# Optimization experiments

Measured on AMD Instinct MI355X. Metric: run time of the kernel, lower is better.

Reference implementation:

```python
import jax, jax.numpy as jnp
import numpy as np
from jax import lax

EPS = 2.220446049250313e-16  # np.finfo(float).eps, as in the torch source
DN3 = ('NCDHW', 'OIDHW', 'NCDHW')
DN2 = ('NCHW', 'OIHW', 'NCHW')


def setup_inputs() -> dict:
    key = jax.random.key(0)
    k1, k2, k3 = jax.random.split(key, 3)
    x = jax.random.normal(k1, (256, 256), dtype=jnp.float32)
    filts_temp = jax.random.normal(k2, (8, 1, 2, 9, 9), dtype=jnp.float32)    # [Ft,1,T=2,kh,kw]
    filts_notemp = jax.random.normal(k3, (8, 1, 1, 9, 9), dtype=jnp.float32)  # [Fn,1,1,kh,kw]
    return {"x": x, "filts_temp": filts_temp, "filts_notemp": filts_notemp, "num_rfs": 2}


def _forward(x, filts_temp, filts_notemp, num_rfs):
    kh, kw = filts_temp.shape[3], filts_temp.shape[4]
    corr_x = num_rfs * kh  # torch uses shape[3]
    corr_y = num_rfs * kw  # torch uses shape[4]
    num_filts = filts_temp.shape[0] + filts_notemp.shape[0]

    # x -> [1,1,2,H,W]: duplicate the frame along a temporal axis of length 2
    xv = jnp.broadcast_to(x, (2,) + x.shape)[None, None]

    # fixed-filter temporal conv3d + ReLU (halved)
    x_temp = jax.nn.relu(
        lax.conv_general_dilated(xv, filts_temp, (1, 1, 1), 'VALID', dimension_numbers=DN3) / 2
    )  # [1,Ft,1,H',W']
    # non-temporal conv on the last time slice
    x_notemp = jax.nn.relu(
        lax.conv_general_dilated(xv[:, :, -1:, :, :], filts_notemp, (1, 1, 1), 'VALID',
                                 dimension_numbers=DN3)
    )  # [1,Fn,1,H',W']

    xc = jnp.concatenate([x_temp, x_notemp], axis=1)  # [1,nf,1,H',W']
    # normalize across the filter channel (divisive normalization)
    x1 = xc / (jnp.sum(xc, axis=1, keepdims=True) + EPS)

    H_, W_ = x1.shape[3], x1.shape[4]
    x1f = x1[0, :, 0]  # [nf,H',W']
    # central crop used as correlation templates
    templates = x1f[:, corr_y:H_ - corr_y, corr_x:W_ - corr_x]  # [nf, H'-2cy, W'-2cx]

    # windowed pairwise cross-channel correlation: the torch conv3d with depth-kernel 1
    # is exactly a batched 2D valid cross-correlation (batch = depth index j,
    # out-channel = template index i)
    out = lax.conv_general_dilated(x1f[:, None], templates[:, None], (1, 1), 'VALID',
                                   dimension_numbers=DN2)  # [j, i, 2cy+1, 2cx+1]
    x2 = jnp.transpose(out, (1, 0, 2, 3))[None]  # [1, i, j, 2cy+1, 2cx+1]
    # note: source divides by (y_max-2*corr_y)*(x_max-2*corr_y) (corr_y twice) -- kept faithful
    x2 = x2 / ((H_ - 2 * corr_y) * (W_ - 2 * corr_y))

    x1_out = x1f[None, None]  # [1,1,nf,H',W']
    return (x1_out, x2)


def reference(x, filts_temp, filts_notemp, num_rfs):
    return _forward(x, filts_temp, filts_notemp, num_rfs)
```

## Files before the change

### kernel.cpp

```cpp
#include <hip/hip_runtime.h>
#include <cstdint>

typedef unsigned short u16;
typedef unsigned int   u32;
typedef unsigned long long u64;
typedef __bf16 bf16x8 __attribute__((ext_vector_type(8)));
typedef float  f32x16 __attribute__((ext_vector_type(16)));
typedef float  f32x4  __attribute__((ext_vector_type(4)));
typedef u32    u32x4  __attribute__((ext_vector_type(4)));

#define OUT1 984064
#define OUT2 350464

#define XD_STRIDE  2031616
#define TMPL_OFFB  16252928
#define PART_OFFB  17801216
#define PART_ELEMS (6*OUT2)
#define XC_OFFB    26212352

__global__ __launch_bounds__(256) void k1_conv(
    const float* __restrict__ x, const float* __restrict__ ft,
    const float* __restrict__ fnt, float* __restrict__ out1,
    u16* __restrict__ Xc) {
  __shared__ float xt[24][25];
  __shared__ float wsm[1296];
  const int tid = threadIdx.x;
  const int lx = tid & 15, ly = tid >> 4;
  const int bx = blockIdx.x, by = blockIdx.y;
  for (int idx = tid; idx < 1296; idx += 256) {
    int c = idx / 81, s = idx - (idx / 81) * 81;
    wsm[idx] = (c < 8) ? 0.5f * (ft[c*162 + s] + ft[c*162 + 81 + s])
                       : fnt[(c-8)*81 + s];
  }
  for (int idx = tid; idx < 576; idx += 256) {
    int ry = idx / 24, rx = idx - ry * 24;
    int gy = by*16 + ry; gy = gy > 255 ? 255 : gy;
    int gx = bx*16 + rx; gx = gx > 255 ? 255 : gx;
    xt[ry][rx] = x[gy*256 + gx];
  }
  __syncthreads();
  const int xg = bx*16 + lx, yg = by*16 + ly;
  if (yg >= 248) return;
  float s[16];
#pragma unroll
  for (int c = 0; c < 16; ++c) s[c] = 0.f;
  const bool valid = (xg < 248);
  if (valid) {
#pragma unroll
    for (int u = 0; u < 9; ++u)
#pragma unroll
      for (int v = 0; v < 9; ++v) {
        float xv = xt[ly + u][lx + v];
#pragma unroll
        for (int c = 0; c < 16; ++c)
          s[c] = __builtin_fmaf(xv, wsm[c*81 + u*9 + v], s[c]);
      }
    float sum = 2.2204460492503131e-16f;
#pragma unroll
    for (int c = 0; c < 16; ++c) { s[c] = s[c] > 0.f ? s[c] : 0.f; sum += s[c]; }
    float inv = 1.f / sum;
#pragma unroll
    for (int c = 0; c < 16; ++c) s[c] *= inv;
  }
#pragma unroll
  for (int c = 0; c < 16; ++c) {
    u16 hb = 0;
    if (valid) {
      out1[c*61504 + yg*248 + xg] = s[c];
      u32 ub = __builtin_bit_cast(u32, s[c]);
      hb = (u16)((ub + 0x7fffu + ((ub >> 16) & 1u)) >> 16);
    }
    if (xg < 264) Xc[(c*248 + yg)*264 + xg] = hb;
  }
}

__global__ __launch_bounds__(256) void k1b_expand(
    const u16* __restrict__ Xc, u16* __restrict__ ws16, float* __restrict__ partial) {
  const int cid = blockIdx.x*256 + threadIdx.x;
  for (int z = cid; z < PART_ELEMS; z += 4346*256) partial[z] = 0.f;
  const u32* src = (const u32*)Xc;
  if (cid < 1015808) {
    int n  = cid & 15;
    int r1 = cid >> 4;
    int row = r1 % 248;
    int r2  = r1 / 248;
    int vb  = r2 & 31;
    int d   = r2 >> 5;
    int colb = (d & ~1) + 8*vb;
    int so = (n*248 + row)*132 + (colb >> 1);
    u32 a0 = src[so], a1 = src[so+1], a2 = src[so+2], a3 = src[so+3], a4 = src[so+4];
    u32x4 v;
    if (d & 1) {
      v[0] = (a0 >> 16) | (a1 << 16); v[1] = (a1 >> 16) | (a2 << 16);
      v[2] = (a2 >> 16) | (a3 << 16); v[3] = (a3 >> 16) | (a4 << 16);
    } else { v[0] = a0; v[1] = a1; v[2] = a2; v[3] = a3; }
    *(u32x4*)(ws16 + (size_t)cid*8) = v;
  } else if (cid < 1015808 + 96768) {
    int t  = cid - 1015808;
    int o  = t & 15;
    int r1 = t >> 4;
    int tr = r1 % 216;
    int vb = r1 / 216;
    u32x4 v = {0u, 0u, 0u, 0u};
    if (tr < 212 && vb < 27) {
      int so = (o*248 + tr + 18)*132 + ((18 + 8*vb) >> 1);
      v[0] = src[so]; v[1] = src[so+1]; v[2] = src[so+2]; v[3] = src[so+3];
      if (vb == 26) { v[2] = 0u; v[3] = 0u; }
    }
    *(u32x4*)(ws16 + (size_t)(TMPL_OFFB/2) + (size_t)t*8) = v;
  }
}

#define F_LD(k,m,c) fl[(k)*1024 + (((m)&3) + 4*((m)>>3))*64 + ((c) + 32*(((m)>>2)&1))]

#define LOADA(DST,q,SO) asm volatile("buffer_load_dwordx4 %0, %1, %2, %3 offen" \
  : "=v"(DST[q]) : "v"(voffA[q]), "s"(srdA), "s"(SO));
#define LOADB(DST,t,SO) asm volatile("buffer_load_dwordx4 %0, %1, %2, %3 offen" \
  : "=v"(DST[t]) : "v"(voffB[t]), "s"(srdB), "s"(SO));
#define ISSUE_G0(NA,NB,SA,SB) LOADA(NA,0,SA) LOADA(NA,1,SA) LOADA(NA,2,SA) \
  LOADA(NA,3,SA) LOADA(NA,4,SA) LOADB(NB,0,SB)
#define ISSUE_GT(NA,NB,t,SA,SB) LOADA(NA,4+t,SA) LOADB(NB,t,SB)
#define W6(N,CA,CB) asm volatile("s_waitcnt vmcnt(" #N ")" : "+v"(CA[0]), \
  "+v"(CA[1]),"+v"(CA[2]),"+v"(CA[3]),"+v"(CA[4]),"+v"(CB[0]) :: );
#define W2(N,CA,CB,t) asm volatile("s_waitcnt vmcnt(" #N ")" \
  : "+v"(CA[4+t]),"+v"(CB[t]) :: );
#define MF5(CA,CB,t) { bf16x8 _bb = __builtin_bit_cast(bf16x8, CB[t]); \
  acc[0]=__builtin_amdgcn_mfma_f32_32x32x16_bf16(__builtin_bit_cast(bf16x8,CA[t+0]),_bb,acc[0],0,0,0); \
  acc[1]=__builtin_amdgcn_mfma_f32_32x32x16_bf16(__builtin_bit_cast(bf16x8,CA[t+1]),_bb,acc[1],0,0,0); \
  acc[2]=__builtin_amdgcn_mfma_f32_32x32x16_bf16(__builtin_bit_cast(bf16x8,CA[t+2]),_bb,acc[2],0,0,0); \
  acc[3]=__builtin_amdgcn_mfma_f32_32x32x16_bf16(__builtin_bit_cast(bf16x8,CA[t+3]),_bb,acc[3],0,0,0); \
  acc[4]=__builtin_amdgcn_mfma_f32_32x32x16_bf16(__builtin_bit_cast(bf16x8,CA[t+4]),_bb,acc[4],0,0,0); }
#define HALF_PF(CA,CB,NA,NB,SA,SB) \
  W6(16,CA,CB)   MF5(CA,CB,0) ISSUE_G0(NA,NB,SA,SB) \
  W2(20,CA,CB,1) MF5(CA,CB,1) ISSUE_GT(NA,NB,1,SA,SB) \
  W2(20,CA,CB,2) MF5(CA,CB,2) ISSUE_GT(NA,NB,2,SA,SB) \
  W2(20,CA,CB,3) MF5(CA,CB,3) ISSUE_GT(NA,NB,3,SA,SB) \
  W2(20,CA,CB,4) MF5(CA,CB,4) ISSUE_GT(NA,NB,4,SA,SB) \
  W2(20,CA,CB,5) MF5(CA,CB,5) ISSUE_GT(NA,NB,5,SA,SB) \
  W2(20,CA,CB,6) MF5(CA,CB,6) ISSUE_GT(NA,NB,6,SA,SB) \
  W2(20,CA,CB,7) MF5(CA,CB,7) ISSUE_GT(NA,NB,7,SA,SB) \
  W2(20,CA,CB,8) MF5(CA,CB,8) ISSUE_GT(NA,NB,8,SA,SB)
#define HALF_LAST(CA,CB) \
  W6(16,CA,CB)   MF5(CA,CB,0) \
  W2(14,CA,CB,1) MF5(CA,CB,1) \
  W2(12,CA,CB,2) MF5(CA,CB,2) \
  W2(10,CA,CB,3) MF5(CA,CB,3) \
  W2(8,CA,CB,4)  MF5(CA,CB,4) \
  W2(6,CA,CB,5)  MF5(CA,CB,5) \
  W2(4,CA,CB,6)  MF5(CA,CB,6) \
  W2(2,CA,CB,7)  MF5(CA,CB,7) \
  W2(0,CA,CB,8)  MF5(CA,CB,8)

__global__ __launch_bounds__(256, 2) void k2_corr(
    const u16* __restrict__ Ximg2, const u16* __restrict__ Tmpl2,
    float* __restrict__ partial) {
  __shared__ float fl[5120];
  const int bid = blockIdx.x;
  const int d   = bid & 7;
  const int m0  = bid >> 3;
  const int jq  = m0 % 5;
  const int cmb = m0 / 5;
  const int g   = cmb & 3;
  const int uq  = cmb >> 2;
  const int j   = d + 8*jq;
  if (j >= 37) return;
  const int U0  = 72*uq;
  const int R0  = 10*g + U0;
  const int tid  = threadIdx.x;
  const int lane = tid & 63;
  const int w    = tid >> 6;
  const int fn16 = lane & 15;
  const int fuu  = (lane >> 4) & 1;
  const int fg   = lane >> 5;

  u64 pa = (u64)((const char*)Ximg2 + d*XD_STRIDE + jq*63488);
  u64 pb = (u64)((const char*)Tmpl2);
  u32x4 srdA = { (u32)pa, (u32)(pa >> 32), 0xFFFFFFFFu, 0x00020000u };
  u32x4 srdB = { (u32)pb, (u32)(pb >> 32), 0xFFFFFFFFu, 0x00020000u };
  int voffA[13], voffB[9];
#pragma unroll
  for (int q = 0; q < 13; ++q) {
    int r = R0 + fuu + 18*w + 2*q;
    if (r > 247) r = 247;
    voffA[q] = fg*63488 + fn16*16 + r*256;
  }
#pragma unroll
  for (int t = 0; t < 9; ++t)
    voffB[t] = fg*55296 + fn16*16 + (U0 + fuu + 18*w + 2*t)*256;

  f32x16 acc[5];
#pragma unroll
  for (int k = 0; k < 5; ++k)
#pragma unroll
    for (int q = 0; q < 16; ++q) acc[k][q] = 0.f;

  u32x4 A0[13], B0[9], A1[13], B1[9];
  int z0 = 0;
  ISSUE_G0(A0,B0,z0,z0)
  ISSUE_GT(A0,B0,1,z0,z0) ISSUE_GT(A0,B0,2,z0,z0) ISSUE_GT(A0,B0,3,z0,z0)
  ISSUE_GT(A0,B0,4,z0,z0) ISSUE_GT(A0,B0,5,z0,z0) ISSUE_GT(A0,B0,6,z0,z0)
  ISSUE_GT(A0,B0,7,z0,z0) ISSUE_GT(A0,B0,8,z0,z0)

#pragma unroll 1
  for (int svp = 0; svp < 6; ++svp) {
    int sA1 = (2*svp + 1)*126976, sB1 = (2*svp + 1)*110592;
    int sA2 = (2*svp + 2)*126976, sB2 = (2*svp + 2)*110592;
    HALF_PF(A0,B0, A1,B1, sA1,sB1)
    HALF_PF(A1,B1, A0,B0, sA2,sB2)
  }
  { int sA = 13*126976, sB = 13*110592;
    HALF_PF(A0,B0, A1,B1, sA,sB) }
  HALF_LAST(A1,B1)
  __syncthreads();

  for (int z = tid; z < 5120; z += 256) fl[z] = 0.f;
  __syncthreads();
  for (int ww = 0; ww < 4; ++ww) {
    if (w == ww) {
#pragma unroll
      for (int k = 0; k < 5; ++k) {
        if (!(g == 3 && k == 4)) {
#pragma unroll
          for (int q = 0; q < 16; ++q)
            fl[k*1024 + q*64 + lane] += acc[k][q];
        }
      }
    }
    __syncthreads();
  }

  const int n = (tid >> 4) & 15;
  const int o = tid & 15;
  float* slab = partial + (uq*2 + (g & 1)) * OUT2;
  for (int ii = 0; ii < 11; ++ii) {
    const int i = 10*g - 1 + ii;
    if (i < 0 || i >= 37) continue;
    const int dd = ii - 1;
    float v;
    if (!(dd & 1)) {
      const int k = dd >> 1;
      v = F_LD(k, n, o) + F_LD(k, n+16, o+16);
    } else {
      v = 0.f;
      if (dd >= 1) v += F_LD((dd-1) >> 1, n+16, o);
      const int kr = (dd+1) >> 1;
      if (kr <= 4) v += F_LD(kr, n, o+16);
    }
    slab[(o*16 + n)*1369 + i*37 + j] = v;
  }
}

__global__ __launch_bounds__(256) void k3_reduce(
    const float* __restrict__ partial, float* __restrict__ out2) {
  const int idx = blockIdx.x*256 + threadIdx.x;
  if (idx >= OUT2/4) return;
  f32x4 s = {0.f, 0.f, 0.f, 0.f};
#pragma unroll
  for (int t = 0; t < 6; ++t) {
    f32x4 v = *(const f32x4*)(partial + t*OUT2 + idx*4);
    s[0] += v[0]; s[1] += v[1]; s[2] += v[2]; s[3] += v[3];
  }
  const float sc = 1.0f / 44944.0f;
  s[0] *= sc; s[1] *= sc; s[2] *= sc; s[3] *= sc;
  *(f32x4*)(out2 + idx*4) = s;
}

extern "C" void kernel_launch(void* const* d_in, const int* in_sizes, int n_in,
                              void* d_out, int out_size, void* d_ws, size_t ws_size,
                              hipStream_t stream) {
  (void)in_sizes; (void)n_in; (void)out_size; (void)ws_size;
  const float* x   = (const float*)d_in[0];
  const float* ft  = (const float*)d_in[1];
  const float* fnt = (const float*)d_in[2];
  float* out = (float*)d_out;
  char*  ws  = (char*)d_ws;
  u16*   Ximg2   = (u16*)ws;
  u16*   Tmpl2   = (u16*)(ws + TMPL_OFFB);
  float* partial = (float*)(ws + PART_OFFB);
  u16*   Xc      = (u16*)(ws + XC_OFFB);

  k1_conv<<<dim3(17, 16), 256, 0, stream>>>(x, ft, fnt, out, Xc);
  k1b_expand<<<4346, 256, 0, stream>>>(Xc, (u16*)ws, partial);
  k2_corr<<<480, 256, 0, stream>>>(Ximg2, Tmpl2, partial);
  k3_reduce<<<343, 256, 0, stream>>>(partial, out + OUT1);
}
```

Baseline: 74.81 us.

## Replace double-buffered register prefetch with single rolling buffer in k2_corr

The correlation kernel's main loop drops its two ping-pong register sets (A0/B0, A1/B1) for a single A/B set. Each fragment is reloaded with the next slice's data as soon as its last MFMA has consumed it, and the vmcnt wait thresholds are retuned for the new issue order. This roughly halves the VGPRs held by prefetch buffers, which may ease register pressure or allow more waves. In exchange, the prefetch distance shrinks to within one slice, so load latency has less MFMA work to hide behind.

```diff
diff --git a/kernel.cpp b/kernel.cpp
--- a/kernel.cpp
+++ b/kernel.cpp
@@ -113,43 +113,17 @@
 
 #define F_LD(k,m,c) fl[(k)*1024 + (((m)&3) + 4*((m)>>3))*64 + ((c) + 32*(((m)>>2)&1))]
 
-#define LOADA(DST,q,SO) asm volatile("buffer_load_dwordx4 %0, %1, %2, %3 offen" \
-  : "=v"(DST[q]) : "v"(voffA[q]), "s"(srdA), "s"(SO));
-#define LOADB(DST,t,SO) asm volatile("buffer_load_dwordx4 %0, %1, %2, %3 offen" \
-  : "=v"(DST[t]) : "v"(voffB[t]), "s"(srdB), "s"(SO));
-#define ISSUE_G0(NA,NB,SA,SB) LOADA(NA,0,SA) LOADA(NA,1,SA) LOADA(NA,2,SA) \
-  LOADA(NA,3,SA) LOADA(NA,4,SA) LOADB(NB,0,SB)
-#define ISSUE_GT(NA,NB,t,SA,SB) LOADA(NA,4+t,SA) LOADB(NB,t,SB)
-#define W6(N,CA,CB) asm volatile("s_waitcnt vmcnt(" #N ")" : "+v"(CA[0]), \
-  "+v"(CA[1]),"+v"(CA[2]),"+v"(CA[3]),"+v"(CA[4]),"+v"(CB[0]) :: );
-#define W2(N,CA,CB,t) asm volatile("s_waitcnt vmcnt(" #N ")" \
-  : "+v"(CA[4+t]),"+v"(CB[t]) :: );
-#define MF5(CA,CB,t) { bf16x8 _bb = __builtin_bit_cast(bf16x8, CB[t]); \
-  acc[0]=__builtin_amdgcn_mfma_f32_32x32x16_bf16(__builtin_bit_cast(bf16x8,CA[t+0]),_bb,acc[0],0,0,0); \
-  acc[1]=__builtin_amdgcn_mfma_f32_32x32x16_bf16(__builtin_bit_cast(bf16x8,CA[t+1]),_bb,acc[1],0,0,0); \
-  acc[2]=__builtin_amdgcn_mfma_f32_32x32x16_bf16(__builtin_bit_cast(bf16x8,CA[t+2]),_bb,acc[2],0,0,0); \
-  acc[3]=__builtin_amdgcn_mfma_f32_32x32x16_bf16(__builtin_bit_cast(bf16x8,CA[t+3]),_bb,acc[3],0,0,0); \
-  acc[4]=__builtin_amdgcn_mfma_f32_32x32x16_bf16(__builtin_bit_cast(bf16x8,CA[t+4]),_bb,acc[4],0,0,0); }
-#define HALF_PF(CA,CB,NA,NB,SA,SB) \
-  W6(16,CA,CB)   MF5(CA,CB,0) ISSUE_G0(NA,NB,SA,SB) \
-  W2(20,CA,CB,1) MF5(CA,CB,1) ISSUE_GT(NA,NB,1,SA,SB) \
-  W2(20,CA,CB,2) MF5(CA,CB,2) ISSUE_GT(NA,NB,2,SA,SB) \
-  W2(20,CA,CB,3) MF5(CA,CB,3) ISSUE_GT(NA,NB,3,SA,SB) \
-  W2(20,CA,CB,4) MF5(CA,CB,4) ISSUE_GT(NA,NB,4,SA,SB) \
-  W2(20,CA,CB,5) MF5(CA,CB,5) ISSUE_GT(NA,NB,5,SA,SB) \
-  W2(20,CA,CB,6) MF5(CA,CB,6) ISSUE_GT(NA,NB,6,SA,SB) \
-  W2(20,CA,CB,7) MF5(CA,CB,7) ISSUE_GT(NA,NB,7,SA,SB) \
-  W2(20,CA,CB,8) MF5(CA,CB,8) ISSUE_GT(NA,NB,8,SA,SB)
-#define HALF_LAST(CA,CB) \
-  W6(16,CA,CB)   MF5(CA,CB,0) \
-  W2(14,CA,CB,1) MF5(CA,CB,1) \
-  W2(12,CA,CB,2) MF5(CA,CB,2) \
-  W2(10,CA,CB,3) MF5(CA,CB,3) \
-  W2(8,CA,CB,4)  MF5(CA,CB,4) \
-  W2(6,CA,CB,5)  MF5(CA,CB,5) \
-  W2(4,CA,CB,6)  MF5(CA,CB,6) \
-  W2(2,CA,CB,7)  MF5(CA,CB,7) \
-  W2(0,CA,CB,8)  MF5(CA,CB,8)
+#define LOADA(q,SO) asm volatile("buffer_load_dwordx4 %0, %1, %2, %3 offen" \
+  : "=v"(A[q]) : "v"(voffA[q]), "s"(srdA), "s"(SO));
+#define LOADB(t,SO) asm volatile("buffer_load_dwordx4 %0, %1, %2, %3 offen" \
+  : "=v"(B[t]) : "v"(voffB[t]), "s"(srdB), "s"(SO));
+#define WT(N,X,Y) asm volatile("s_waitcnt vmcnt(" #N ")" : "+v"(X), "+v"(Y) ::);
+#define MF5(t) { bf16x8 _bb = __builtin_bit_cast(bf16x8, B[t]); \
+  acc[0]=__builtin_amdgcn_mfma_f32_32x32x16_bf16(__builtin_bit_cast(bf16x8,A[t+0]),_bb,acc[0],0,0,0); \
+  acc[1]=__builtin_amdgcn_mfma_f32_32x32x16_bf16(__builtin_bit_cast(bf16x8,A[t+1]),_bb,acc[1],0,0,0); \
+  acc[2]=__builtin_amdgcn_mfma_f32_32x32x16_bf16(__builtin_bit_cast(bf16x8,A[t+2]),_bb,acc[2],0,0,0); \
+  acc[3]=__builtin_amdgcn_mfma_f32_32x32x16_bf16(__builtin_bit_cast(bf16x8,A[t+3]),_bb,acc[3],0,0,0); \
+  acc[4]=__builtin_amdgcn_mfma_f32_32x32x16_bf16(__builtin_bit_cast(bf16x8,A[t+4]),_bb,acc[4],0,0,0); }
 
 __global__ __launch_bounds__(256, 2) void k2_corr(
     const u16* __restrict__ Ximg2, const u16* __restrict__ Tmpl2,
@@ -194,23 +168,37 @@
 #pragma unroll
     for (int q = 0; q < 16; ++q) acc[k][q] = 0.f;
 
-  u32x4 A0[13], B0[9], A1[13], B1[9];
-  int z0 = 0;
-  ISSUE_G0(A0,B0,z0,z0)
-  ISSUE_GT(A0,B0,1,z0,z0) ISSUE_GT(A0,B0,2,z0,z0) ISSUE_GT(A0,B0,3,z0,z0)
-  ISSUE_GT(A0,B0,4,z0,z0) ISSUE_GT(A0,B0,5,z0,z0) ISSUE_GT(A0,B0,6,z0,z0)
-  ISSUE_GT(A0,B0,7,z0,z0) ISSUE_GT(A0,B0,8,z0,z0)
+  u32x4 A[13], B[9];
+  { int sa = 0, sb = 0;
+    LOADA(0,sa) LOADB(0,sb) LOADA(1,sa) LOADB(1,sb)
+    LOADA(2,sa) LOADB(2,sb) LOADA(3,sa) LOADB(3,sb)
+    LOADA(4,sa) LOADB(4,sb) LOADA(5,sa) LOADB(5,sb)
+    LOADA(6,sa) LOADB(6,sb) LOADA(7,sa) LOADB(7,sb)
+    LOADA(8,sa) LOADA(9,sa) LOADA(10,sa) LOADA(11,sa) LOADA(12,sa) LOADB(8,sb) }
 
 #pragma unroll 1
-  for (int svp = 0; svp < 6; ++svp) {
-    int sA1 = (2*svp + 1)*126976, sB1 = (2*svp + 1)*110592;
-    int sA2 = (2*svp + 2)*126976, sB2 = (2*svp + 2)*110592;
-    HALF_PF(A0,B0, A1,B1, sA1,sB1)
-    HALF_PF(A1,B1, A0,B0, sA2,sB2)
-  }
-  { int sA = 13*126976, sB = 13*110592;
-    HALF_PF(A0,B0, A1,B1, sA,sB) }
-  HALF_LAST(A1,B1)
+  for (int sv = 0; sv < 13; ++sv) {
+    const int sa = (sv + 1)*126976, sb = (sv + 1)*110592;
+    WT(13, A[4],  B[0])  MF5(0) LOADA(0,sa) LOADB(0,sb)
+    WT(13, A[5],  B[1])  MF5(1) LOADA(1,sa) LOADB(1,sb)
+    WT(13, A[6],  B[2])  MF5(2) LOADA(2,sa) LOADB(2,sb)
+    WT(13, A[7],  B[3])  MF5(3) LOADA(3,sa) LOADB(3,sb)
+    WT(13, A[8],  B[4])  MF5(4) LOADA(4,sa) LOADB(4,sb)
+    WT(14, A[9],  B[5])  MF5(5) LOADA(5,sa) LOADB(5,sb)
+    WT(15, A[10], B[6])  MF5(6) LOADA(6,sa) LOADB(6,sb)
+    WT(16, A[11], B[7])  MF5(7) LOADA(7,sa) LOADB(7,sb)
+    WT(16, A[12], B[8])  MF5(8)
+    LOADA(8,sa) LOADA(9,sa) LOADA(10,sa) LOADA(11,sa) LOADA(12,sa) LOADB(8,sb)
+  }
+  WT(13, A[4],  B[0])  MF5(0)
+  WT(11, A[5],  B[1])  MF5(1)
+  WT(9,  A[6],  B[2])  MF5(2)
+  WT(7,  A[7],  B[3])  MF5(3)
+  WT(5,  A[8],  B[4])  MF5(4)
+  WT(4,  A[9],  B[5])  MF5(5)
+  WT(3,  A[10], B[6])  MF5(6)
+  WT(2,  A[11], B[7])  MF5(7)
+  WT(0,  A[12], B[8])  MF5(8)
   __syncthreads();
 
   for (int z = tid; z < 5120; z += 256) fl[z] = 0.f;
```

Measured after the change: 74.54 us. No clear change (-0.4%).
